# Optimization experiments

Hardware: AMD Instinct MI355X
Metric: run time of the kernel (lower is better)

Reference implementation:

```python
import jax, jax.numpy as jnp
import numpy as np

EMBED = 1024
HEADS = 16
DIM_HEAD = EMBED // HEADS
N, L = 4, 2048


def setup_inputs() -> dict:
    key = jax.random.key(0)
    ks = jax.random.split(key, 12)
    s = 0.02
    return {
        "q": jax.random.normal(ks[0], (N, L, EMBED), jnp.float32),
        "k": jax.random.normal(ks[1], (N, L, EMBED), jnp.float32),
        "v": jax.random.normal(ks[2], (N, L, EMBED), jnp.float32),
        "padding_mask": jnp.ones((N, L), dtype=bool),
        "sequence_mask": jnp.zeros((L, L), dtype=bool),
        # Linear(in, out): store weight as [out, in] like torch, bias [out]
        "Wq": jax.random.normal(ks[3], (EMBED, EMBED), jnp.float32) * s,
        "bq": jnp.zeros((EMBED,), jnp.float32),
        "Wk": jax.random.normal(ks[4], (EMBED, EMBED), jnp.float32) * s,
        "bk": jnp.zeros((EMBED,), jnp.float32),
        "Wv": jax.random.normal(ks[5], (EMBED, EMBED), jnp.float32) * s,
        "bv": jnp.zeros((EMBED,), jnp.float32),
        "Wo": jax.random.normal(ks[6], (EMBED, EMBED), jnp.float32) * s,
        "bo": jnp.zeros((EMBED,), jnp.float32),
    }


def reference(q, k, v, padding_mask, sequence_mask, Wq, bq, Wk, bk, Wv, bv, Wo, bo):
    n, lq, _ = q.shape
    lk = k.shape[1]
    # input projections
    qp = (q @ Wq.T + bq).reshape(n, lq, HEADS, DIM_HEAD)
    kp = (k @ Wk.T + bk).reshape(n, lk, HEADS, DIM_HEAD)
    vp = (v @ Wv.T + bv).reshape(n, lk, HEADS, DIM_HEAD)
    # energy: [n, h, lq, lk]
    energy = jnp.einsum('nqhd,nkhd->nhqk', qp, kp)
    attention = jax.nn.softmax(energy / jnp.sqrt(jnp.float32(EMBED)), axis=3)
    # NOTE: the original torch code calls masked_fill (non in-place) and
    # discards the result, so padding_mask / sequence_mask have NO effect.
    # Dropout is also never applied in forward. Replicated faithfully.
    out = jnp.einsum('nhqk,nkhd->nqhd', attention, vp)
    out = out.reshape(n, lq, EMBED)
    return out @ Wo.T + bo
```

## Files before the change

kernel.cpp:

```cpp
#include <hip/hip_runtime.h>
#include <stdint.h>

typedef _Float16 f16;
typedef _Float16 f16x8 __attribute__((ext_vector_type(8)));
typedef _Float16 f16x4 __attribute__((ext_vector_type(4)));
typedef _Float16 f16x2 __attribute__((ext_vector_type(2)));
typedef float f32x4 __attribute__((ext_vector_type(4)));

__device__ __forceinline__ f32x4 mfma16(f16x8 a, f16x8 b, f32x4 c) {
    return __builtin_amdgcn_mfma_f32_16x16x32_f16(a, b, c, 0, 0, 0);
}

__device__ __forceinline__ void gload16(const f16* g, f16* l) {
    __builtin_amdgcn_global_load_lds(
        (const __attribute__((address_space(1))) uint32_t*)g,
        (__attribute__((address_space(3))) uint32_t*)l, 16, 0, 0);
}

template <bool OUT16>
__device__ __forceinline__ void gemm_body(const f16* __restrict__ A,
                                          const f16* __restrict__ B,
                                          const float* __restrict__ bias,
                                          void* __restrict__ Cout, long ldo,
                                          int biasrow, float scale,
                                          long m0, long n0, f16* As, f16* Bs) {
    int tid = threadIdx.x;
    int lane = tid & 63, w = tid >> 6;
    int wm = w & 1, wn = w >> 1;
    int l15 = lane & 15, quad = lane >> 4;

    int rg = lane >> 3;
    int cg = (lane & 7) ^ rg;
    const f16* ag[4];
    const f16* bg[4];
    f16* al[4];
    f16* bl[4];
#pragma unroll
    for (int t = 0; t < 4; ++t) {
        int rb = (w * 4 + t) * 8;
        ag[t] = A + (m0 + rb + rg) * 1024 + cg * 8;
        bg[t] = B + (n0 + rb + rg) * 1024 + cg * 8;
        al[t] = &As[rb * 64];
        bl[t] = &Bs[rb * 64];
    }

    f32x4 acc[4][4] = {};

    for (int k0 = 0; k0 < 1024; k0 += 64) {
        __syncthreads();
#pragma unroll
        for (int t = 0; t < 4; ++t) {
            gload16(ag[t] + k0, al[t]);
            gload16(bg[t] + k0, bl[t]);
        }
        __syncthreads();
#pragma unroll
        for (int ks = 0; ks < 2; ++ks) {
            int cc = (ks * 4 + quad) ^ (l15 & 7);
            f16x8 af[4], bf[4];
#pragma unroll
            for (int t = 0; t < 4; ++t) {
                af[t] = *(const f16x8*)&As[(wm * 64 + t * 16 + l15) * 64 + cc * 8];
                bf[t] = *(const f16x8*)&Bs[(wn * 64 + t * 16 + l15) * 64 + cc * 8];
            }
#pragma unroll
            for (int i = 0; i < 4; ++i)
#pragma unroll
                for (int j = 0; j < 4; ++j)
                    acc[i][j] = mfma16(af[i], bf[j], acc[i][j]);
        }
    }

#pragma unroll
    for (int i = 0; i < 4; ++i) {
        int mrow = wm * 64 + i * 16 + quad * 4;
#pragma unroll
        for (int j = 0; j < 4; ++j) {
            int ncol = wn * 64 + j * 16 + l15;
            long gn = n0 + ncol;
#pragma unroll
            for (int r = 0; r < 4; ++r) {
                long gm = m0 + mrow + r;
                float v = (acc[i][j][r] + (biasrow ? bias[gm] : bias[gn])) * scale;
                if constexpr (OUT16)
                    ((f16*)Cout)[gm * ldo + gn] = (f16)v;
                else
                    ((float*)Cout)[gm * ldo + gn] = v;
            }
        }
    }
}

__global__ __launch_bounds__(256, 2) void qkv_proj(
    const f16* __restrict__ qh, const f16* __restrict__ kh,
    const f16* __restrict__ vh, const f16* __restrict__ Wh,
    const float* __restrict__ bq, const float* __restrict__ bk,
    const float* __restrict__ bv, f16* __restrict__ Qp, f16* __restrict__ Kp,
    f16* __restrict__ Vt) {
    __shared__ __align__(16) f16 As[128 * 64];
    __shared__ __align__(16) f16 Bs[128 * 64];
    int z = blockIdx.z;
    const f16* A;
    const f16* B;
    const float* bias;
    f16* C;
    long ldo;
    int biasrow;
    float scale;
    if (z == 0) {
        A = qh; B = Wh; bias = bq; C = Qp; ldo = 1024; biasrow = 0;
        scale = 0.0450842200277786f;
    } else if (z == 1) {
        A = kh; B = Wh + 1048576; bias = bk; C = Kp; ldo = 1024; biasrow = 0;
        scale = 1.0f;
    } else {
        A = Wh + 2097152; B = vh; bias = bv; C = Vt; ldo = 8192; biasrow = 1;
        scale = 1.0f;
    }
    long m0 = (long)(z == 2 ? blockIdx.y : blockIdx.x) * 128;
    long n0 = (long)(z == 2 ? blockIdx.x : blockIdx.y) * 128;
    gemm_body<true>(A, B, bias, C, ldo, biasrow, scale, m0, n0, As, Bs);
}

__global__ __launch_bounds__(256, 2) void o_proj(const f16* __restrict__ Op,
                                                 const f16* __restrict__ Wo,
                                                 const float* __restrict__ bo,
                                                 float* __restrict__ out) {
    __shared__ __align__(16) f16 As[128 * 64];
    __shared__ __align__(16) f16 Bs[128 * 64];
    gemm_body<false>(Op, Wo, bo, out, 1024, 0, 1.0f, (long)blockIdx.x * 128,
                     (long)blockIdx.y * 128, As, Bs);
}

__global__ __launch_bounds__(256, 2) void attn256(const f16* __restrict__ Qp,
                                                  const f16* __restrict__ Kp,
                                                  const f16* __restrict__ Vt,
                                                  f16* __restrict__ Op) {
    __shared__ __align__(16) f16 Ps0[128 * 64];
    __shared__ __align__(16) f16 Ps1[128 * 64];
    __shared__ __align__(16) f16 Ks[2][64 * 64];
    __shared__ __align__(16) f16 Vs[2][64 * 64];

    int tid = threadIdx.x;
    int lane = tid & 63, w = tid >> 6;
    int l15 = lane & 15, quad = lane >> 4;
    int b = blockIdx.x;
    int xcd = b & 7, slot = b >> 3;
    int nh = xcd * 8 + (slot >> 3);
    int qp = slot & 7;
    int nb = nh >> 4, h = nh & 15;
    long tok0 = (long)nb * 2048;
    long qrow0 = qp * 256;

    int rg = lane >> 3, cg = (lane & 7) ^ rg;

    const f16* qsrc0 = Qp + (tok0 + qrow0) * 1024 + h * 64;
    const f16* qsrc1 = qsrc0 + 128 * 1024;
#pragma unroll
    for (int t = 0; t < 4; ++t) {
        int rb = w * 32 + t * 8;
        gload16(qsrc0 + (rb + rg) * 1024 + cg * 8, &Ps0[rb * 64]);
        gload16(qsrc1 + (rb + rg) * 1024 + cg * 8, &Ps1[rb * 64]);
    }
    const f16* kptr = Kp + (tok0 + w * 16 + rg) * 1024 + h * 64 + cg * 8;
    const f16* vptr = Vt + ((long)h * 64 + w * 16 + rg) * 8192 + tok0 + cg * 8;
    gload16(kptr, &Ks[0][(w * 16) * 64]);
    gload16(kptr + 8 * 1024, &Ks[0][(w * 16 + 8) * 64]);
    gload16(vptr, &Vs[0][(w * 16) * 64]);
    gload16(vptr + (long)8 * 8192, &Vs[0][(w * 16 + 8) * 64]);
    const f16* kn = kptr + 65536;
    const f16* vn = vptr + 64;
    __syncthreads();

    f16x8 qf0[2][2], qf1[2][2];
#pragma unroll
    for (int ks = 0; ks < 2; ++ks) {
        int cc = (ks * 4 + quad) ^ (l15 & 7);
#pragma unroll
        for (int j = 0; j < 2; ++j) {
            qf0[ks][j] = *(const f16x8*)&Ps0[(w * 32 + j * 16 + l15) * 64 + cc * 8];
            qf1[ks][j] = *(const f16x8*)&Ps1[(w * 32 + j * 16 + l15) * 64 + cc * 8];
        }
    }

    f32x4 oacc0[2][4] = {}, oacc1[2][4] = {};
    float rs0[2] = {0.f, 0.f}, rs1[2] = {0.f, 0.f};
    const f32x4 z4 = {0.f, 0.f, 0.f, 0.f};

    for (int kt = 0; kt < 32; ++kt) {
        int cur = kt & 1;
        f32x4 sacc0[4][2], sacc1[4][2];
#pragma unroll
        for (int ks = 0; ks < 2; ++ks) {
            int cc = (ks * 4 + quad) ^ (l15 & 7);
            f16x8 a[4];
#pragma unroll
            for (int t = 0; t < 4; ++t)
                a[t] = *(const f16x8*)&Ks[cur][(t * 16 + l15) * 64 + cc * 8];
#pragma unroll
            for (int i = 0; i < 4; ++i)
#pragma unroll
                for (int j = 0; j < 2; ++j) {
                    if (ks == 0) {
                        sacc0[i][j] = mfma16(a[i], qf0[0][j], z4);
                        sacc1[i][j] = mfma16(a[i], qf1[0][j], z4);
                    } else {
                        sacc0[i][j] = mfma16(a[i], qf0[1][j], sacc0[i][j]);
                        sacc1[i][j] = mfma16(a[i], qf1[1][j], sacc1[i][j]);
                    }
                }
        }
        if (kt < 31) {
            int nxt = cur ^ 1;
            f16* kd = &Ks[nxt][(w * 16) * 64];
            f16* vd = &Vs[nxt][(w * 16) * 64];
            gload16(kn, kd);
            gload16(kn + 8 * 1024, kd + 8 * 64);
            gload16(vn, vd);
            gload16(vn + (long)8 * 8192, vd + 8 * 64);
            kn += 65536;
            vn += 64;
        }
#pragma unroll
        for (int i = 0; i < 4; ++i) {
#pragma unroll
            for (int j = 0; j < 2; ++j) {
                int qrow = w * 32 + j * 16 + l15;
                int kl = i * 16 + quad * 4;
                int c = kl >> 3;
                int off = qrow * 64 + ((c ^ (qrow & 7)) << 3) + (kl & 7);
                {
                    float p0 = __builtin_amdgcn_exp2f(sacc0[i][j][0]);
                    float p1 = __builtin_amdgcn_exp2f(sacc0[i][j][1]);
                    float p2 = __builtin_amdgcn_exp2f(sacc0[i][j][2]);
                    float p3 = __builtin_amdgcn_exp2f(sacc0[i][j][3]);
                    rs0[j] += (p0 + p1) + (p2 + p3);
                    f16x2 lo = __builtin_bit_cast(f16x2, __builtin_amdgcn_cvt_pkrtz(p0, p1));
                    f16x2 hi = __builtin_bit_cast(f16x2, __builtin_amdgcn_cvt_pkrtz(p2, p3));
                    f16x4 ph;
                    ph[0] = lo[0]; ph[1] = lo[1]; ph[2] = hi[0]; ph[3] = hi[1];
                    *(f16x4*)&Ps0[off] = ph;
                }
                {
                    float p0 = __builtin_amdgcn_exp2f(sacc1[i][j][0]);
                    float p1 = __builtin_amdgcn_exp2f(sacc1[i][j][1]);
                    float p2 = __builtin_amdgcn_exp2f(sacc1[i][j][2]);
                    float p3 = __builtin_amdgcn_exp2f(sacc1[i][j][3]);
                    rs1[j] += (p0 + p1) + (p2 + p3);
                    f16x2 lo = __builtin_bit_cast(f16x2, __builtin_amdgcn_cvt_pkrtz(p0, p1));
                    f16x2 hi = __builtin_bit_cast(f16x2, __builtin_amdgcn_cvt_pkrtz(p2, p3));
                    f16x4 ph;
                    ph[0] = lo[0]; ph[1] = lo[1]; ph[2] = hi[0]; ph[3] = hi[1];
                    *(f16x4*)&Ps1[off] = ph;
                }
            }
        }
#pragma unroll
        for (int ks = 0; ks < 2; ++ks) {
            int cc = (ks * 4 + quad) ^ (l15 & 7);
            f16x8 bf[4];
#pragma unroll
            for (int j = 0; j < 4; ++j)
                bf[j] = *(const f16x8*)&Vs[cur][(j * 16 + l15) * 64 + cc * 8];
            f16x8 af0[2], af1[2];
#pragma unroll
            for (int i = 0; i < 2; ++i) {
                af0[i] = *(const f16x8*)&Ps0[(w * 32 + i * 16 + l15) * 64 + cc * 8];
                af1[i] = *(const f16x8*)&Ps1[(w * 32 + i * 16 + l15) * 64 + cc * 8];
            }
#pragma unroll
            for (int i = 0; i < 2; ++i)
#pragma unroll
                for (int j = 0; j < 4; ++j) {
                    oacc0[i][j] = mfma16(af0[i], bf[j], oacc0[i][j]);
                    oacc1[i][j] = mfma16(af1[i], bf[j], oacc1[i][j]);
                }
        }
        __syncthreads();
    }

    float* lsi = (float*)&Ks[0][0];
#pragma unroll
    for (int j = 0; j < 2; ++j) {
        rs0[j] += __shfl_xor(rs0[j], 16, 64);
        rs0[j] += __shfl_xor(rs0[j], 32, 64);
        rs1[j] += __shfl_xor(rs1[j], 16, 64);
        rs1[j] += __shfl_xor(rs1[j], 32, 64);
    }
    if (lane < 16) {
        lsi[w * 32 + lane] = 1.0f / rs0[0];
        lsi[w * 32 + 16 + lane] = 1.0f / rs0[1];
        lsi[128 + w * 32 + lane] = 1.0f / rs1[0];
        lsi[128 + w * 32 + 16 + lane] = 1.0f / rs1[1];
    }

    long otok = tok0 + qrow0;
#pragma unroll
    for (int i = 0; i < 2; ++i) {
        int qrow = w * 32 + i * 16 + quad * 4;
#pragma unroll
        for (int j = 0; j < 4; ++j) {
            int d = j * 16 + l15;
#pragma unroll
            for (int r = 0; r < 4; ++r) {
                Op[(otok + qrow + r) * 1024 + h * 64 + d] =
                    (f16)(oacc0[i][j][r] * lsi[qrow + r]);
                Op[(otok + 128 + qrow + r) * 1024 + h * 64 + d] =
                    (f16)(oacc1[i][j][r] * lsi[128 + qrow + r]);
            }
        }
    }
}

__global__ void cvt_all(const float* __restrict__ q, const float* __restrict__ k,
                        const float* __restrict__ v, const float* __restrict__ w0,
                        const float* __restrict__ w1, const float* __restrict__ w2,
                        const float* __restrict__ w3, f16* __restrict__ qh,
                        f16* __restrict__ kh, f16* __restrict__ vh,
                        f16* __restrict__ wh) {
    long id = (long)blockIdx.x * 256 + threadIdx.x;
    const float* s;
    f16* d;
    long off;
    if (id < 3145728) {
        int which = (int)(id >> 20);
        off = (id & 1048575) * 8;
        s = which == 0 ? q : which == 1 ? k : v;
        d = which == 0 ? qh : which == 1 ? kh : vh;
    } else {
        long id2 = id - 3145728;
        int wi = (int)(id2 >> 17);
        off = (id2 & 131071) * 8;
        s = wi == 0 ? w0 : wi == 1 ? w1 : wi == 2 ? w2 : w3;
        d = wh + (long)wi * 1048576;
    }
    f32x4 a = *(const f32x4*)(s + off);
    f32x4 b = *(const f32x4*)(s + off + 4);
    f16x8 hv;
    hv[0] = (f16)a[0]; hv[1] = (f16)a[1]; hv[2] = (f16)a[2]; hv[3] = (f16)a[3];
    hv[4] = (f16)b[0]; hv[5] = (f16)b[1]; hv[6] = (f16)b[2]; hv[7] = (f16)b[3];
    *(f16x8*)(d + off) = hv;
}

extern "C" void kernel_launch(void* const* d_in, const int* in_sizes, int n_in,
                              void* d_out, int out_size, void* d_ws, size_t ws_size,
                              hipStream_t stream) {
    const float* q  = (const float*)d_in[0];
    const float* k  = (const float*)d_in[1];
    const float* v  = (const float*)d_in[2];
    const float* Wq = (const float*)d_in[5];
    const float* bq = (const float*)d_in[6];
    const float* Wk = (const float*)d_in[7];
    const float* bk = (const float*)d_in[8];
    const float* Wv = (const float*)d_in[9];
    const float* bv = (const float*)d_in[10];
    const float* Wo = (const float*)d_in[11];
    const float* bo = (const float*)d_in[12];

    char* ws = (char*)d_ws;
    f16* qh = (f16*)ws;
    f16* kh = (f16*)(ws + (16L << 20));
    f16* vh = (f16*)(ws + (32L << 20));
    f16* Wh = (f16*)(ws + (48L << 20));
    f16* Qp = (f16*)(ws + (56L << 20));
    f16* Kp = (f16*)(ws + (72L << 20));
    f16* Vt = (f16*)(ws + (88L << 20));
    f16* Op = (f16*)(ws + (104L << 20));

    cvt_all<<<14336, 256, 0, stream>>>(q, k, v, Wq, Wk, Wv, Wo, qh, kh, vh, Wh);

    qkv_proj<<<dim3(64, 8, 3), 256, 0, stream>>>(qh, kh, vh, Wh, bq, bk, bv,
                                                 Qp, Kp, Vt);

    attn256<<<512, 256, 0, stream>>>(Qp, Kp, Vt, Op);

    o_proj<<<dim3(64, 8), 256, 0, stream>>>(Op, Wh + 3145728, bo, (float*)d_out);
}
```

Measured before the change: 340.2 us.

## Triple-buffer GEMM and attention K/V tiles with vmcnt-based single-barrier pipelining

The projection GEMMs move from a two-barrier synchronous loop with 64-wide K tiles to a three-stage ring of 32-wide K tiles. Loads are issued two steps ahead, with partial s_waitcnt vmcnt and one raw s_barrier per step. The attention kernel likewise goes from double- to triple-buffered K/V tiles, replaces __syncthreads with counted waits, and adds s_setprio around the MFMA sections. The aim is to hide global-to-LDS latency behind MFMA work, at the cost of more LDS, which may reduce occupancy, and fragile hand-counted wait counts.

```diff
diff --git a/kernel.cpp b/kernel.cpp
--- a/kernel.cpp
+++ b/kernel.cpp
@@ -29,46 +29,69 @@
     int wm = w & 1, wn = w >> 1;
     int l15 = lane & 15, quad = lane >> 4;
 
-    int rg = lane >> 3;
-    int cg = (lane & 7) ^ rg;
-    const f16* ag[4];
-    const f16* bg[4];
-    f16* al[4];
-    f16* bl[4];
-#pragma unroll
-    for (int t = 0; t < 4; ++t) {
-        int rb = (w * 4 + t) * 8;
-        ag[t] = A + (m0 + rb + rg) * 1024 + cg * 8;
-        bg[t] = B + (n0 + rb + rg) * 1024 + cg * 8;
-        al[t] = &As[rb * 64];
-        bl[t] = &Bs[rb * 64];
+    int r4 = lane >> 2;
+    int c4 = (lane & 3) ^ ((lane >> 3) & 3);
+    const f16* ag[2];
+    const f16* bg[2];
+    int off[2];
+#pragma unroll
+    for (int t = 0; t < 2; ++t) {
+        int rb = t * 64 + w * 16;
+        ag[t] = A + (m0 + rb + r4) * 1024 + c4 * 8;
+        bg[t] = B + (n0 + rb + r4) * 1024 + c4 * 8;
+        off[t] = rb * 32;
     }
 
     f32x4 acc[4][4] = {};
 
-    for (int k0 = 0; k0 < 1024; k0 += 64) {
-        __syncthreads();
+#pragma unroll
+    for (int t = 0; t < 2; ++t) {
+        gload16(ag[t], &As[off[t]]);
+        gload16(bg[t], &Bs[off[t]]);
+    }
+#pragma unroll
+    for (int t = 0; t < 2; ++t) {
+        gload16(ag[t] + 32, &As[4096 + off[t]]);
+        gload16(bg[t] + 32, &Bs[4096 + off[t]]);
+    }
+    asm volatile("s_waitcnt vmcnt(4)" ::: "memory");
+    __builtin_amdgcn_s_barrier();
+    __builtin_amdgcn_sched_barrier(0);
+
+    int cur = 0;
+    for (int kt = 0; kt < 32; ++kt) {
+        if (kt < 30) {
+            int slot = (cur == 0) ? 2 : cur - 1;
+            const int ko = (kt + 2) * 32;
+#pragma unroll
+            for (int t = 0; t < 2; ++t) {
+                gload16(ag[t] + ko, &As[slot * 4096 + off[t]]);
+                gload16(bg[t] + ko, &Bs[slot * 4096 + off[t]]);
+            }
+        }
+        const f16* as = As + cur * 4096;
+        const f16* bs = Bs + cur * 4096;
+        int cs = (quad ^ ((l15 >> 1) & 3)) * 8;
+        f16x8 af[4], bf[4];
 #pragma unroll
         for (int t = 0; t < 4; ++t) {
-            gload16(ag[t] + k0, al[t]);
-            gload16(bg[t] + k0, bl[t]);
-        }
-        __syncthreads();
-#pragma unroll
-        for (int ks = 0; ks < 2; ++ks) {
-            int cc = (ks * 4 + quad) ^ (l15 & 7);
-            f16x8 af[4], bf[4];
-#pragma unroll
-            for (int t = 0; t < 4; ++t) {
-                af[t] = *(const f16x8*)&As[(wm * 64 + t * 16 + l15) * 64 + cc * 8];
-                bf[t] = *(const f16x8*)&Bs[(wn * 64 + t * 16 + l15) * 64 + cc * 8];
-            }
-#pragma unroll
-            for (int i = 0; i < 4; ++i)
-#pragma unroll
-                for (int j = 0; j < 4; ++j)
-                    acc[i][j] = mfma16(af[i], bf[j], acc[i][j]);
-        }
+            af[t] = *(const f16x8*)&as[(wm * 64 + t * 16 + l15) * 32 + cs];
+            bf[t] = *(const f16x8*)&bs[(wn * 64 + t * 16 + l15) * 32 + cs];
+        }
+#pragma unroll
+        for (int i = 0; i < 4; ++i)
+#pragma unroll
+            for (int j = 0; j < 4; ++j)
+                acc[i][j] = mfma16(af[i], bf[j], acc[i][j]);
+        if (kt < 31) {
+            if (kt < 30)
+                asm volatile("s_waitcnt vmcnt(4)" ::: "memory");
+            else
+                asm volatile("s_waitcnt vmcnt(0)" ::: "memory");
+            __builtin_amdgcn_s_barrier();
+            __builtin_amdgcn_sched_barrier(0);
+        }
+        cur = (cur == 2) ? 0 : cur + 1;
     }
 
 #pragma unroll
@@ -97,8 +120,8 @@
     const float* __restrict__ bq, const float* __restrict__ bk,
     const float* __restrict__ bv, f16* __restrict__ Qp, f16* __restrict__ Kp,
     f16* __restrict__ Vt) {
-    __shared__ __align__(16) f16 As[128 * 64];
-    __shared__ __align__(16) f16 Bs[128 * 64];
+    __shared__ __align__(16) f16 As[3 * 128 * 32];
+    __shared__ __align__(16) f16 Bs[3 * 128 * 32];
     int z = blockIdx.z;
     const f16* A;
     const f16* B;
@@ -126,8 +149,8 @@
                                                  const f16* __restrict__ Wo,
                                                  const float* __restrict__ bo,
                                                  float* __restrict__ out) {
-    __shared__ __align__(16) f16 As[128 * 64];
-    __shared__ __align__(16) f16 Bs[128 * 64];
+    __shared__ __align__(16) f16 As[3 * 128 * 32];
+    __shared__ __align__(16) f16 Bs[3 * 128 * 32];
     gemm_body<false>(Op, Wo, bo, out, 1024, 0, 1.0f, (long)blockIdx.x * 128,
                      (long)blockIdx.y * 128, As, Bs);
 }
@@ -138,8 +161,8 @@
                                                   f16* __restrict__ Op) {
     __shared__ __align__(16) f16 Ps0[128 * 64];
     __shared__ __align__(16) f16 Ps1[128 * 64];
-    __shared__ __align__(16) f16 Ks[2][64 * 64];
-    __shared__ __align__(16) f16 Vs[2][64 * 64];
+    __shared__ __align__(16) f16 Ks[3][64 * 64];
+    __shared__ __align__(16) f16 Vs[3][64 * 64];
 
     int tid = threadIdx.x;
     int lane = tid & 63, w = tid >> 6;
@@ -168,10 +191,14 @@
     gload16(kptr + 8 * 1024, &Ks[0][(w * 16 + 8) * 64]);
     gload16(vptr, &Vs[0][(w * 16) * 64]);
     gload16(vptr + (long)8 * 8192, &Vs[0][(w * 16 + 8) * 64]);
-    const f16* kn = kptr + 65536;
-    const f16* vn = vptr + 64;
-    __syncthreads();
-
+    gload16(kptr + 65536, &Ks[1][(w * 16) * 64]);
+    gload16(kptr + 65536 + 8 * 1024, &Ks[1][(w * 16 + 8) * 64]);
+    gload16(vptr + 64, &Vs[1][(w * 16) * 64]);
+    gload16(vptr + 64 + (long)8 * 8192, &Vs[1][(w * 16 + 8) * 64]);
+    const f16* kn = kptr + 2 * 65536;
+    const f16* vn = vptr + 2 * 64;
+
+    asm volatile("s_waitcnt vmcnt(8)" ::: "memory");
     f16x8 qf0[2][2], qf1[2][2];
 #pragma unroll
     for (int ks = 0; ks < 2; ++ks) {
@@ -182,14 +209,18 @@
             qf1[ks][j] = *(const f16x8*)&Ps1[(w * 32 + j * 16 + l15) * 64 + cc * 8];
         }
     }
+    asm volatile("s_waitcnt vmcnt(4)" ::: "memory");
+    __builtin_amdgcn_s_barrier();
+    __builtin_amdgcn_sched_barrier(0);
 
     f32x4 oacc0[2][4] = {}, oacc1[2][4] = {};
     float rs0[2] = {0.f, 0.f}, rs1[2] = {0.f, 0.f};
     const f32x4 z4 = {0.f, 0.f, 0.f, 0.f};
 
+    int cur = 0;
     for (int kt = 0; kt < 32; ++kt) {
-        int cur = kt & 1;
         f32x4 sacc0[4][2], sacc1[4][2];
+        __builtin_amdgcn_s_setprio(1);
 #pragma unroll
         for (int ks = 0; ks < 2; ++ks) {
             int cc = (ks * 4 + quad) ^ (l15 & 7);
@@ -210,8 +241,9 @@
                     }
                 }
         }
-        if (kt < 31) {
-            int nxt = cur ^ 1;
+        __builtin_amdgcn_s_setprio(0);
+        if (kt < 30) {
+            int nxt = (cur == 0) ? 2 : cur - 1;
             f16* kd = &Ks[nxt][(w * 16) * 64];
             f16* vd = &Vs[nxt][(w * 16) * 64];
             gload16(kn, kd);
@@ -255,6 +287,7 @@
                 }
             }
         }
+        __builtin_amdgcn_s_setprio(1);
 #pragma unroll
         for (int ks = 0; ks < 2; ++ks) {
             int cc = (ks * 4 + quad) ^ (l15 & 7);
@@ -272,11 +305,20 @@
             for (int i = 0; i < 2; ++i)
 #pragma unroll
                 for (int j = 0; j < 4; ++j) {
-                    oacc0[i][j] = mfma16(af0[i], bf[j], oacc0[i][j]);
+                    oacc0[i][j] = mfma16(af0[i], bf[ks * 0 + j], oacc0[i][j]);
                     oacc1[i][j] = mfma16(af1[i], bf[j], oacc1[i][j]);
                 }
         }
-        __syncthreads();
+        __builtin_amdgcn_s_setprio(0);
+        if (kt < 31) {
+            if (kt < 30)
+                asm volatile("s_waitcnt vmcnt(4)" ::: "memory");
+            else
+                asm volatile("s_waitcnt vmcnt(0)" ::: "memory");
+            __builtin_amdgcn_s_barrier();
+            __builtin_amdgcn_sched_barrier(0);
+        }
+        cur = (cur == 2) ? 0 : cur + 1;
     }
 
     float* lsi = (float*)&Ks[0][0];
```

Result: no change. 340.5 us (+0.1%).
